# Kernel tuning notes

Measured on AMD Instinct MI355X. Metric: run time of the kernel, lower is better.

The kernel has to match this reference:

```python
import jax, jax.numpy as jnp
import numpy as np

K_SIM_SCHEDULE = [4, 8, 16]
K_CON_SCHEDULE = [2, 4, 8]
NEG = 1000000000.0


def _dual_adjacency(h, k_sim, k_con):
    """Binary causal dual adjacency (similar / dissimilar), no gradient."""
    B, T, D = h.shape
    h = jax.lax.stop_gradient(h)
    xn = h / jnp.maximum(jnp.linalg.norm(h, axis=-1, keepdims=True), 1e-12)
    sim = jnp.einsum('btd,bsd->bts', xn, xn)                 # (B,T,T)
    past = jnp.tril(jnp.ones((T, T), h.dtype), -1)           # strictly-past mask
    sim = sim * past - NEG * (1.0 - past)
    eff_sim = min(k_sim, T - 1)
    eff_con = min(k_con, max(0, T - 1 - eff_sim))
    bI = jnp.arange(B)[:, None, None]
    tI = jnp.arange(T)[None, :, None]
    A_sim = jnp.zeros((B, T, T), h.dtype)
    if eff_sim > 0:
        _, top_idx = jax.lax.top_k(sim, eff_sim)             # (B,T,k)
        A_sim = A_sim.at[bI, tI, top_idx].set(1.0) * past
    A_con = jnp.zeros((B, T, T), h.dtype)
    if eff_con > 0:
        sim_con = jnp.where(A_sim > 0, NEG, sim)
        _, bot_idx = jax.lax.top_k(-sim_con, eff_con)        # smallest eff_con
        A_con = A_con.at[bI, tI, bot_idx].set(1.0) * past * (1.0 - A_sim)
    return A_sim, A_con


def _aggregate(h, A):
    # unweighted mean over selected neighbors; empty rows -> zeros
    deg = jnp.sum(A, axis=-1, keepdims=True)
    return jnp.einsum('bts,bsd->btd', A, h) / jnp.maximum(deg, 1.0)


def setup_inputs() -> dict:
    key = jax.random.key(0)
    ks = jax.random.split(key, 2)
    B, T, D, R = 4, 2048, 512, 3
    x = jax.random.normal(ks[0], (B, T, D), dtype=jnp.float32)
    gain = jnp.ones((R, D), dtype=jnp.float32)
    bias = jnp.zeros((R, D), dtype=jnp.float32)
    log_mix = jnp.zeros((R,), dtype=jnp.float32)
    log_alpha = jnp.zeros((R,), dtype=jnp.float32)
    log_momentum = jnp.asarray(1.0, dtype=jnp.float32)
    log_scale = jnp.asarray(0.0, dtype=jnp.float32)
    return {"x": x, "gain": gain, "bias": bias, "log_mix": log_mix,
            "log_alpha": log_alpha, "log_momentum": log_momentum,
            "log_scale": log_scale}


def reference(x, gain, bias, log_mix, log_alpha, log_momentum, log_scale):
    momentum = jax.nn.sigmoid(log_momentum)
    scale = jax.nn.softplus(log_scale) + 0.01
    h = x
    for r in range(len(K_SIM_SCHEDULE)):
        mix = jax.nn.sigmoid(log_mix[r])
        alpha = jax.nn.sigmoid(log_alpha[r])
        A_sim, A_con = _dual_adjacency(h, K_SIM_SCHEDULE[r], K_CON_SCHEDULE[r])
        msg_pos = _aggregate(h, A_sim)
        msg_neg = _aggregate(h, A_con)
        ctx = alpha * msg_pos + (1.0 - alpha) * msg_neg
        blended = mix * h + (1.0 - mix) * ctx
        h_new = jax.nn.gelu(blended * gain[r] + bias[r], approximate=False)
        h = momentum * h + (1.0 - momentum) * h_new
    return (h - x) * scale
```

## Files before the change

### kernel.cpp

```cpp
#include <hip/hip_runtime.h>
#include <hip/hip_bf16.h>
#include <cstdint>
#include <cstddef>

#define BB 4
#define TT 2048
#define DD 512
#define NEG_INF (-3.402823466e+38f)
#define POS_INF (3.402823466e+38f)

typedef __attribute__((ext_vector_type(8))) short bf16x8;
typedef __attribute__((ext_vector_type(8))) unsigned short ushort8;
typedef __attribute__((ext_vector_type(4))) float f32x4;

__device__ __forceinline__ float sigmoidf_(float x){ return 1.0f/(1.0f+expf(-x)); }

__device__ __forceinline__ unsigned short f2bf(float x){
  __hip_bfloat16 b = __float2bfloat16(x);
  return *reinterpret_cast<unsigned short*>(&b);
}

__device__ __forceinline__ unsigned int fwd_map(float f){
  unsigned int b = __float_as_uint(f);
  return b ^ ((b & 0x80000000u) ? 0xFFFFFFFFu : 0x80000000u);
}
__device__ __forceinline__ float inv_map(unsigned int u){
  unsigned int b = (u & 0x80000000u) ? (u ^ 0x80000000u) : ~u;
  return __uint_as_float(b);
}

__device__ __forceinline__ unsigned long long shfl_xor64(unsigned long long x, int off){
  unsigned int hi = __shfl_xor((unsigned int)(x >> 32), off);
  unsigned int lo = __shfl_xor((unsigned int)x, off);
  return ((unsigned long long)hi << 32) | lo;
}

__global__ __launch_bounds__(64) void k_normsplit(const float* __restrict__ h, float* __restrict__ rnorm,
                                                  unsigned short* __restrict__ Xh, unsigned short* __restrict__ Xl){
  int row = blockIdx.x;
  const float* hr = h + (size_t)row*DD;
  int lane = threadIdx.x;
  float4 v0 = *(const float4*)&hr[lane*4];
  float4 v1 = *(const float4*)&hr[lane*4 + 256];
  float ss = v0.x*v0.x+v0.y*v0.y+v0.z*v0.z+v0.w*v0.w
           + v1.x*v1.x+v1.y*v1.y+v1.z*v1.z+v1.w*v1.w;
  #pragma unroll
  for (int off=32; off; off>>=1) ss += __shfl_xor(ss, off);
  float rn = 1.0f / fmaxf(sqrtf(ss), 1e-12f);
  if (lane==0) rnorm[row] = rn;

  float xs[8] = {v0.x,v0.y,v0.z,v0.w,v1.x,v1.y,v1.z,v1.w};
  unsigned short hb[8], lb[8];
  #pragma unroll
  for (int q=0;q<8;q++){
    float xn = xs[q]*rn;
    unsigned short hh = f2bf(xn);
    __hip_bfloat16 bh = *reinterpret_cast<__hip_bfloat16*>(&hh);
    float rem = xn - __bfloat162float(bh);
    hb[q] = hh; lb[q] = f2bf(rem);
  }
  ushort4 h0 = {hb[0],hb[1],hb[2],hb[3]}, h1 = {hb[4],hb[5],hb[6],hb[7]};
  ushort4 l0 = {lb[0],lb[1],lb[2],lb[3]}, l1 = {lb[4],lb[5],lb[6],lb[7]};
  *(ushort4*)&Xh[(size_t)row*DD + lane*4]       = h0;
  *(ushort4*)&Xh[(size_t)row*DD + lane*4 + 256] = h1;
  *(ushort4*)&Xl[(size_t)row*DD + lane*4]       = l0;
  *(ushort4*)&Xl[(size_t)row*DD + lane*4 + 256] = l1;
}

__global__ __launch_bounds__(256) void k_sim(const unsigned short* __restrict__ Xh,
                                             const unsigned short* __restrict__ Xl,
                                             float* __restrict__ sim, int b0){
  int p = blockIdx.x;
  int jt = (int)((sqrtf(8.0f*(float)p + 1.0f) - 1.0f)*0.5f);
  while ((jt+1)*(jt+2)/2 <= p) jt++;
  while (jt*(jt+1)/2 > p) jt--;
  int is = p - jt*(jt+1)/2;

  int bl = blockIdx.y;
  size_t xoff = (size_t)(b0 + bl)*TT*DD;
  const unsigned short* XhB = Xh + xoff;
  const unsigned short* XlB = Xl + xoff;
  float* simb = sim + (size_t)bl*TT*TT;
  int t0 = jt*128, s0 = is*128;

  __shared__ __align__(16) short As[128*32];
  __shared__ __align__(16) short Bs[128*32];

  int tid = threadIdx.x, wave = tid>>6, lane = tid&63;
  int wr = wave>>1, wc = wave&1;

  int srow = tid>>2;
  int sc8  = (tid&3)*8;

  f32x4 acc[4][4];
  #pragma unroll
  for (int m=0;m<4;m++)
    #pragma unroll
    for (int n=0;n<4;n++) acc[m][n] = (f32x4){0.f,0.f,0.f,0.f};

  ushort8 ra0, ra1, rb0, rb1;
  auto gload = [&](int s){
    int pass = s>>4; int kcol = (s&15)*32;
    const unsigned short* sA = (pass<2) ? XhB : XlB;
    const unsigned short* sB = (pass!=1) ? XhB : XlB;
    ra0 = *(const ushort8*)&sA[(size_t)(t0+srow)*DD + kcol + sc8];
    ra1 = *(const ushort8*)&sA[(size_t)(t0+srow+64)*DD + kcol + sc8];
    rb0 = *(const ushort8*)&sB[(size_t)(s0+srow)*DD + kcol + sc8];
    rb1 = *(const ushort8*)&sB[(size_t)(s0+srow+64)*DD + kcol + sc8];
  };

  gload(0);
  for (int s=0; s<48; ++s){
    __syncthreads();
    *(ushort8*)&As[srow*32 + sc8]      = ra0;
    *(ushort8*)&As[(srow+64)*32 + sc8] = ra1;
    *(ushort8*)&Bs[srow*32 + sc8]      = rb0;
    *(ushort8*)&Bs[(srow+64)*32 + sc8] = rb1;
    __syncthreads();
    if (s < 47) gload(s+1);

    int arow = wr*64 + (lane&15);
    int brow = wc*64 + (lane&15);
    int kb = (lane>>4)*8;
    bf16x8 af[4], bf[4];
    #pragma unroll
    for (int m=0;m<4;m++) af[m] = *(const bf16x8*)&As[(arow + m*16)*32 + kb];
    #pragma unroll
    for (int n=0;n<4;n++) bf[n] = *(const bf16x8*)&Bs[(brow + n*16)*32 + kb];
    #pragma unroll
    for (int m=0;m<4;m++)
      #pragma unroll
      for (int n=0;n<4;n++)
        acc[m][n] = __builtin_amdgcn_mfma_f32_16x16x32_bf16(af[m], bf[n], acc[m][n], 0, 0, 0);
  }

  #pragma unroll
  for (int m=0;m<4;m++){
    int t = t0 + wr*64 + m*16 + (lane>>4)*4;
    #pragma unroll
    for (int n=0;n<4;n++){
      int sc = s0 + wc*64 + n*16 + (lane&15);
      float* dst = simb + (size_t)t*TT + sc;
      #pragma unroll
      for (int j=0;j<4;j++) dst[(size_t)j*TT] = acc[m][n][j];
    }
  }
}

#define BMASK 0xFFFFFF00u

__device__ __forceinline__ unsigned int radix24(const float* __restrict__ srow, int t, int k1,
                                                unsigned int flip, int* sh, int lane){
  #pragma unroll
  for (int i=0;i<4;i++) sh[lane + i*64] = 0;
  int t4 = t & ~3;
  for (int s4 = lane*4; s4 < t4; s4 += 256){
    float4 f = *(const float4*)&srow[s4];
    unsigned int u0=fwd_map(f.x)^flip, u1=fwd_map(f.y)^flip, u2=fwd_map(f.z)^flip, u3=fwd_map(f.w)^flip;
    atomicAdd(&sh[u0>>24],1); atomicAdd(&sh[u1>>24],1);
    atomicAdd(&sh[u2>>24],1); atomicAdd(&sh[u3>>24],1);
  }
  for (int s = t4 + lane; s < t; s += 64){
    unsigned int u = fwd_map(srow[s])^flip;
    atomicAdd(&sh[u>>24],1);
  }
  unsigned int pfx = 0u; int kp = k1;
  #pragma unroll
  for (int pass = 0; pass < 3; ++pass){
    int shift = 24 - 8*pass;
    int m4 = sh[4*lane] + sh[4*lane+1] + sh[4*lane+2] + sh[4*lane+3];
    int x = __shfl(m4, 63-lane);
    #pragma unroll
    for (int off = 1; off < 64; off <<= 1){
      int v = __shfl_up(x, off);
      if (lane >= off) x += v;
    }
    int T = __shfl(x, 63-lane);
    int G = T - m4;
    bool hit = (G < kp) && (kp <= T);
    unsigned int npfx = 0u; int nkp = 0;
    if (hit){
      int c = G; int D = 4*lane;
      #pragma unroll
      for (int i = 3; i >= 0; --i){
        int hc = sh[4*lane + i];
        if (kp <= c + hc){ D = 4*lane + i; break; }
        c += hc;
      }
      npfx = pfx | ((unsigned int)D << shift);
      nkp = kp - c;
    }
    unsigned long long hm = __ballot(hit);
    int src = __ffsll(hm) - 1;
    pfx = __shfl(npfx, src);
    kp  = __shfl(nkp, src);
    if (pass == 2) break;

    int nshift = shift - 8;
    unsigned int keep = 0xFFFFFFFFu << shift;
    #pragma unroll
    for (int i=0;i<4;i++) sh[lane + i*64] = 0;
    for (int s4 = lane*4; s4 < t4; s4 += 256){
      float4 f = *(const float4*)&srow[s4];
      unsigned int u0=fwd_map(f.x)^flip, u1=fwd_map(f.y)^flip, u2=fwd_map(f.z)^flip, u3=fwd_map(f.w)^flip;
      if (((u0 ^ pfx) & keep) == 0) atomicAdd(&sh[(u0>>nshift)&255],1);
      if (((u1 ^ pfx) & keep) == 0) atomicAdd(&sh[(u1>>nshift)&255],1);
      if (((u2 ^ pfx) & keep) == 0) atomicAdd(&sh[(u2>>nshift)&255],1);
      if (((u3 ^ pfx) & keep) == 0) atomicAdd(&sh[(u3>>nshift)&255],1);
    }
    for (int s = t4 + lane; s < t; s += 64){
      unsigned int u = fwd_map(srow[s])^flip;
      if (((u ^ pfx) & keep) == 0) atomicAdd(&sh[(u>>nshift)&255],1);
    }
  }
  return pfx;
}

template<int ESIM, int ECON>
__global__ __launch_bounds__(256) void k_topk(const float* __restrict__ sim, int b0,
                                              const float* __restrict__ h, const float* __restrict__ rnorm,
                                              int* __restrict__ topidx, int* __restrict__ botidx,
                                              int* __restrict__ bcnt){
  constexpr int K1  = ESIM + 8;
  constexpr int K1B = ESIM + ECON + 8;
  constexpr int CANDCAP = 40;
  constexpr int EQCAP = 44;
  constexpr float TAU = 5e-5f;
  __shared__ int s_hist[4][256];
  __shared__ int s_cand[4][CANDCAP];
  __shared__ int s_eq[4][EQCAP];
  __shared__ int s_sel[4][ESIM];
  __shared__ int s_bot[4][16];
  __shared__ int s_cnt[4][2];

  int tid = threadIdx.x, lane = tid & 63, wid = tid >> 6;
  int lrow = blockIdx.x*4 + wid;
  int bl = lrow >> 11, t = lrow & (TT-1);
  int gb = b0 + bl;
  int grow = (gb << 11) | t;

  if (t <= ESIM){
    if (lane < t) topidx[(size_t)grow*16 + lane] = lane;
    if (lane == 0) bcnt[grow] = 0;
    return;
  }
  const float* srow = sim + (size_t)lrow*TT;
  const float* hb  = h + (size_t)gb*TT*DD;
  const float* rnb = rnorm + (size_t)gb*TT;

  int* sh    = s_hist[wid];
  int* scand = s_cand[wid];
  int* seq   = s_eq[wid];
  int* ssel  = s_sel[wid];
  int* sbot  = s_bot[wid];
  int t4 = t & ~3;

  unsigned long long kv0=0, kv1=0, kv2=0, kv3=0;
  {
    #define MKKEY(F,S) ((((unsigned long long)fwd_map(F)) << 32) | (unsigned int)(~(S)))
    #define INS(KK) do{ unsigned long long a=(KK); \
      if (a > kv3){ \
        if (a > kv0){ unsigned long long tq=kv0; kv0=a; a=tq; } \
        if (a > kv1){ unsigned long long tq=kv1; kv1=a; a=tq; } \
        if (a > kv2){ unsigned long long tq=kv2; kv2=a; a=tq; } \
        kv3=a; } }while(0)
    for (int s4 = lane*4; s4 < t4; s4 += 256){
      float4 f = *(const float4*)&srow[s4];
      INS(MKKEY(f.x,s4)); INS(MKKEY(f.y,s4+1)); INS(MKKEY(f.z,s4+2)); INS(MKKEY(f.w,s4+3));
    }
    for (int s = t4 + lane; s < t; s += 64) INS(MKKEY(srow[s],s));
  }

  int myidx = 0x7fffffff;
  float vA = 0.f, vB = 0.f;
  unsigned long long keyLast = 0ull;
  #pragma unroll
  for (int k = 0; k <= ESIM; ++k){
    unsigned long long bk = kv0;
    #pragma unroll
    for (int off=32; off; off>>=1){
      unsigned long long ok = shfl_xor64(bk, off);
      if (ok > bk) bk = ok;
    }
    if (kv0 == bk){ kv0=kv1; kv1=kv2; kv2=kv3; kv3=0ull; }
    if (lane == k) myidx = (int)(~(unsigned int)bk);
    if (k == ESIM-1) vA = inv_map((unsigned int)(bk >> 32));
    if (k == ESIM){ vB = inv_map((unsigned int)(bk >> 32)); keyLast = bk; }
  }

  int cnt = 0;
  for (int s4 = lane*4; s4 < t4; s4 += 256){
    float4 f = *(const float4*)&srow[s4];
    cnt += (MKKEY(f.x,s4)   > keyLast);
    cnt += (MKKEY(f.y,s4+1) > keyLast);
    cnt += (MKKEY(f.z,s4+2) > keyLast);
    cnt += (MKKEY(f.w,s4+3) > keyLast);
  }
  for (int s = t4 + lane; s < t; s += 64) cnt += (MKKEY(srow[s],s) > keyLast);
  #pragma unroll
  for (int off=32; off; off>>=1) cnt += __shfl_xor(cnt, off);

  bool fb = (cnt != ESIM) || (vA - vB < TAU);
  if (!fb){
    if (lane < ESIM){
      ssel[lane] = myidx;
      topidx[(size_t)grow*16 + lane] = myidx;
    }
  } else {
    int k1 = min(t, K1);
    unsigned int thr = radix24(srow, t, k1, 0u, sh, lane);

    if (lane == 0){ s_cnt[wid][0] = 0; s_cnt[wid][1] = 0; }
    for (int s4 = lane*4; s4 < t4; s4 += 256){
      float4 f = *(const float4*)&srow[s4];
      unsigned int uu[4] = {fwd_map(f.x), fwd_map(f.y), fwd_map(f.z), fwd_map(f.w)};
      #pragma unroll
      for (int q=0;q<4;q++){
        unsigned int b24 = uu[q] & BMASK;
        if (b24 > thr){ int p = atomicAdd(&s_cnt[wid][0],1); if (p < CANDCAP) scand[p] = s4+q; }
        else if (b24 == thr){ int p = atomicAdd(&s_cnt[wid][1],1); if (p < EQCAP) seq[p] = s4+q; }
      }
    }
    for (int s = t4 + lane; s < t; s += 64){
      unsigned int b24 = fwd_map(srow[s]) & BMASK;
      if (b24 > thr){ int p = atomicAdd(&s_cnt[wid][0],1); if (p < CANDCAP) scand[p] = s; }
      else if (b24 == thr){ int p = atomicAdd(&s_cnt[wid][1],1); if (p < EQCAP) seq[p] = s; }
    }
    int c_gt = min(s_cnt[wid][0], CANDCAP);
    int c_eq = min(s_cnt[wid][1], EQCAP);
    int ncand = min(c_gt + c_eq, 64);

    unsigned int myu = 0u; int myi = 0x7fffffff;
    if (lane < ncand){
      myi = (lane < c_gt) ? scand[lane] : seq[lane - c_gt];
      myu = fwd_map(srow[myi]);
    }

    float fvA = 0.f, fvB = 0.f;
    {
      unsigned int cu = myu; int ci = myi;
      #pragma unroll
      for (int k = 0; k <= ESIM; ++k){
        unsigned int bu = cu; int bi = ci;
        #pragma unroll
        for (int off=32; off; off>>=1){
          unsigned int ou = __shfl_xor(bu, off); int oi = __shfl_xor(bi, off);
          if (ou > bu || (ou == bu && oi < bi)){ bu = ou; bi = oi; }
        }
        if (k < ESIM && lane == 0) ssel[k] = bi;
        if (k == ESIM-1) fvA = inv_map(bu);
        if (k == ESIM)   fvB = inv_map(bu);
        if (ci == bi){ cu = 0u; ci = 0x7fffffff; }
      }
    }

    bool resc = (fvA - fvB < TAU);
    if (resc){
      const float* hq = hb + (size_t)t*DD;
      float rt = rnb[t];
      float4 q0 = *(const float4*)&hq[lane*4];
      float4 q1 = *(const float4*)&hq[lane*4 + 256];
      float ev = NEG_INF;
      for (int j = 0; j < ncand; ++j){
        int idx = (j < c_gt) ? scand[j] : seq[j - c_gt];
        const float* hc = hb + (size_t)idx*DD;
        float4 c0 = *(const float4*)&hc[lane*4];
        float4 c1 = *(const float4*)&hc[lane*4 + 256];
        float pp = q0.x*c0.x+q0.y*c0.y+q0.z*c0.z+q0.w*c0.w
                 + q1.x*c1.x+q1.y*c1.y+q1.z*c1.z+q1.w*c1.w;
        #pragma unroll
        for (int off=32; off; off>>=1) pp += __shfl_xor(pp, off);
        float ex = pp * rt * rnb[idx];
        if (lane == j) ev = ex;
      }
      float rv = (lane < ncand) ? ev : NEG_INF;
      int   ri = myi;
      #pragma unroll
      for (int k = 0; k < ESIM; ++k){
        float bv = rv; int bi = ri;
        #pragma unroll
        for (int off=32; off; off>>=1){
          float ov = __shfl_xor(bv, off); int oi = __shfl_xor(bi, off);
          if (ov > bv || (ov == bv && oi < bi)){ bv = ov; bi = oi; }
        }
        if (lane == 0) ssel[k] = bi;
        if (ri == bi) rv = NEG_INF;
      }
    }
    if (lane < ESIM) topidx[(size_t)grow*16 + lane] = ssel[lane];
  }

  int need = ECON - (TT - t);
  int cnt2 = 0;
  if (need > 0){
    constexpr unsigned int FLIP = 0xFFFFFFFFu;
    int k1b = min(t, K1B);
    unsigned int thrb = radix24(srow, t, k1b, FLIP, sh, lane);

    if (lane == 0){ s_cnt[wid][0] = 0; s_cnt[wid][1] = 0; }
    for (int s4 = lane*4; s4 < t4; s4 += 256){
      float4 f = *(const float4*)&srow[s4];
      unsigned int uu[4] = {fwd_map(f.x)^FLIP, fwd_map(f.y)^FLIP, fwd_map(f.z)^FLIP, fwd_map(f.w)^FLIP};
      #pragma unroll
      for (int q=0;q<4;q++){
        unsigned int b24 = uu[q] & BMASK;
        if (b24 > thrb){ int p = atomicAdd(&s_cnt[wid][0],1); if (p < CANDCAP) scand[p] = s4+q; }
        else if (b24 == thrb){ int p = atomicAdd(&s_cnt[wid][1],1); if (p < EQCAP) seq[p] = s4+q; }
      }
    }
    for (int s = t4 + lane; s < t; s += 64){
      unsigned int u = fwd_map(srow[s])^FLIP;
      unsigned int b24 = u & BMASK;
      if (b24 > thrb){ int p = atomicAdd(&s_cnt[wid][0],1); if (p < CANDCAP) scand[p] = s; }
      else if (b24 == thrb){ int p = atomicAdd(&s_cnt[wid][1],1); if (p < EQCAP) seq[p] = s; }
    }
    int bc_gt = min(s_cnt[wid][0], CANDCAP);
    int bc_eq = min(s_cnt[wid][1], EQCAP);
    int ncb = min(bc_gt + bc_eq, 64);

    unsigned int mu = 0u; int mi = 0x7fffffff;
    if (lane < ncb){
      mi = (lane < bc_gt) ? scand[lane] : seq[lane - bc_gt];
      mu = fwd_map(srow[mi]) ^ FLIP;
    }
    float wA = 0.f, wB = 0.f;
    unsigned int cu = mu; int ci = mi;
    #pragma unroll
    for (int k = 0; k < K1B; ++k){
      if (k < ncb && cnt2 < need + 8){
        unsigned int bu = cu; int bi = ci;
        #pragma unroll
        for (int off=32; off; off>>=1){
          unsigned int ou = __shfl_xor(bu, off); int oi = __shfl_xor(bi, off);
          if (ou > bu || (ou == bu && oi < bi)){ bu = ou; bi = oi; }
        }
        if (ci == bi){ cu = 0u; ci = 0x7fffffff; }
        bool mem = false;
        #pragma unroll
        for (int j=0;j<ESIM;j++) if (ssel[j] == bi) mem = true;
        if (!mem){
          if (lane == 0) sbot[cnt2] = bi;
          float val = inv_map(bu ^ FLIP);
          if (cnt2 == need-1) wA = val;
          if (cnt2 == need)   wB = val;
          cnt2++;
        }
      }
    }
    int npick = min(need, cnt2);
    bool rb = (cnt2 > need) && (wB - wA < TAU);
    if (!rb){
      if (lane < npick) botidx[(size_t)grow*8 + lane] = sbot[lane];
    } else {
      const float* hq = hb + (size_t)t*DD;
      float rt = rnb[t];
      float4 q0 = *(const float4*)&hq[lane*4];
      float4 q1 = *(const float4*)&hq[lane*4 + 256];
      float ev = POS_INF; int ei = 0x7fffffff;
      for (int j = 0; j < cnt2; ++j){
        int idx = sbot[j];
        const float* hc = hb + (size_t)idx*DD;
        float4 c0 = *(const float4*)&hc[lane*4];
        float4 c1 = *(const float4*)&hc[lane*4 + 256];
        float pp = q0.x*c0.x+q0.y*c0.y+q0.z*c0.z+q0.w*c0.w
                 + q1.x*c1.x+q1.y*c1.y+q1.z*c1.z+q1.w*c1.w;
        #pragma unroll
        for (int off=32; off; off>>=1) pp += __shfl_xor(pp, off);
        float ex = pp * rt * rnb[idx];
        if (lane == j){ ev = ex; ei = idx; }
      }
      #pragma unroll
      for (int k = 0; k < ECON; ++k){
        if (k < npick){
          float bv = ev; int bi = ei;
          #pragma unroll
          for (int off=32; off; off>>=1){
            float ov = __shfl_xor(bv, off); int oi = __shfl_xor(bi, off);
            if (ov < bv || (ov == bv && oi < bi)){ bv = ov; bi = oi; }
          }
          if (lane == 0) botidx[(size_t)grow*8 + k] = bi;
          if (ei == bi) ev = POS_INF;
        }
      }
    }
    cnt2 = npick;
  }
  if (lane == 0) bcnt[grow] = cnt2;
}

__global__ __launch_bounds__(256) void k_agg(const float* __restrict__ hsrc, float* __restrict__ hdst,
                                             const int* __restrict__ topidx, const int* __restrict__ botidx,
                                             const int* __restrict__ bcnt,
                                             const float* __restrict__ gain, const float* __restrict__ bias,
                                             const float* __restrict__ log_mix, const float* __restrict__ log_alpha,
                                             const float* __restrict__ log_momentum, int r, int eff_sim){
  int row = blockIdx.x;
  int b = row >> 11; int t = row & (TT-1);
  int n_sim = min(eff_sim, t);
  int n_con = bcnt[row];
  float mix      = sigmoidf_(log_mix[r]);
  float alpha    = sigmoidf_(log_alpha[r]);
  float momentum = sigmoidf_(log_momentum[0]);
  const float* hb = hsrc + (size_t)b*TT*DD;

  __shared__ int sidx[16];
  __shared__ int scidx[8];
  if (threadIdx.x < 16) sidx[threadIdx.x]  = (threadIdx.x < n_sim) ? topidx[(size_t)row*16 + threadIdx.x] : 0;
  if (threadIdx.x < 8)  scidx[threadIdx.x] = (threadIdx.x < n_con) ? botidx[(size_t)row*8  + threadIdx.x] : 0;
  __syncthreads();

  #pragma unroll
  for (int e = threadIdx.x; e < DD; e += 256){
    float sp = 0.f;
    for (int j=0;j<n_sim;j++) sp += hb[(size_t)sidx[j]*DD + e];
    float sn = 0.f;
    for (int j=0;j<n_con;j++) sn += hb[(size_t)scidx[j]*DD + e];
    float mp = sp / (float)max(n_sim, 1);
    float mn = sn / (float)max(n_con, 1);
    float ctx = alpha*mp + (1.f-alpha)*mn;
    float hv = hsrc[(size_t)row*DD + e];
    float blended = mix*hv + (1.f-mix)*ctx;
    float u = blended*gain[e] + bias[e];
    float g = 0.5f*u*(1.0f + erff(u*0.7071067811865475f));
    hdst[(size_t)row*DD + e] = momentum*hv + (1.f-momentum)*g;
  }
}

__global__ __launch_bounds__(256) void k_final(const float* __restrict__ hfin, const float* __restrict__ x,
                                               const float* __restrict__ log_scale, float* __restrict__ out, int n){
  float scale = log1pf(expf(log_scale[0])) + 0.01f;
  int i = blockIdx.x*256 + threadIdx.x;
  if (i < n) out[i] = (hfin[i] - x[i]) * scale;
}

extern "C" void kernel_launch(void* const* d_in, const int* in_sizes, int n_in,
                              void* d_out, int out_size, void* d_ws, size_t ws_size,
                              hipStream_t stream) {
  const float* x         = (const float*)d_in[0];
  const float* gain      = (const float*)d_in[1];
  const float* bias      = (const float*)d_in[2];
  const float* log_mix   = (const float*)d_in[3];
  const float* log_alpha = (const float*)d_in[4];
  const float* log_mom   = (const float*)d_in[5];
  const float* log_scale = (const float*)d_in[6];

  float* hA = (float*)d_out;
  char* ws = (char*)d_ws;
  size_t off = 0;
  auto alloc = [&](size_t bytes){ void* p = ws + off; off += (bytes + 255) & ~(size_t)255; return p; };

  float*          hB     = (float*)alloc((size_t)BB*TT*DD*4);
  float*          rnorm  = (float*)alloc((size_t)BB*TT*4);
  int*            topidx = (int*)  alloc((size_t)BB*TT*16*4);
  int*            botidx = (int*)  alloc((size_t)BB*TT*8*4);
  int*            bcnt   = (int*)  alloc((size_t)BB*TT*4);
  unsigned short* Xh     = (unsigned short*)alloc((size_t)BB*TT*DD*2);
  unsigned short* Xl     = (unsigned short*)alloc((size_t)BB*TT*DD*2);

  size_t rem = (ws_size > off) ? (ws_size - off) : 0;
  int cb = (int)(rem / ((size_t)TT*TT*4));
  if (cb < 1) cb = 1;
  if (cb > BB) cb = BB;
  float* sim = (float*)alloc((size_t)cb*TT*TT*4);

  const float* hsrc = x;
  float* hdst = hB;
  const int ks[3] = {4, 8, 16};

  for (int r = 0; r < 3; ++r){
    k_normsplit<<<BB*TT, 64, 0, stream>>>(hsrc, rnorm, Xh, Xl);
    for (int b0 = 0; b0 < BB; b0 += cb){
      int nb = (BB - b0 < cb) ? (BB - b0) : cb;
      dim3 g(136, nb);
      k_sim<<<g, 256, 0, stream>>>(Xh, Xl, sim, b0);
      if (r == 0)      k_topk<4,2><<<nb*TT/4, 256, 0, stream>>>(sim, b0, hsrc, rnorm, topidx, botidx, bcnt);
      else if (r == 1) k_topk<8,4><<<nb*TT/4, 256, 0, stream>>>(sim, b0, hsrc, rnorm, topidx, botidx, bcnt);
      else             k_topk<16,8><<<nb*TT/4, 256, 0, stream>>>(sim, b0, hsrc, rnorm, topidx, botidx, bcnt);
    }
    k_agg<<<BB*TT, 256, 0, stream>>>(hsrc, hdst, topidx, botidx, bcnt,
                                     gain + (size_t)r*DD, bias + (size_t)r*DD,
                                     log_mix, log_alpha, log_mom, r, ks[r]);
    if (r == 0){ hsrc = hB; hdst = hA; }
    else if (r == 1){ hsrc = hA; hdst = hB; }
  }
  k_final<<<(BB*TT*DD)/256, 256, 0, stream>>>(hB, x, log_scale, (float*)d_out, BB*TT*DD);
}
```

Before: 462.9 us.

## Process each top-k row with a full 256-thread block instead of one wave

The top-k kernel now assigns one similarity row per block, with all four waves scanning the row for the candidate pass and the verification count. Each wave publishes its local top-(k+1) keys to shared memory, wave 0 merges them, and the count is combined through a shared atomic. The fallback radix path and the bottom-k selection remain single-wave, so the other three waves sit idle there. This adds block-wide syncs and launches four times as many blocks in exchange for shorter per-row scan latency.

```diff
diff --git a/kernel.cpp b/kernel.cpp
--- a/kernel.cpp
+++ b/kernel.cpp
@@ -148,6 +148,13 @@
 }
 
 #define BMASK 0xFFFFFF00u
+#define MKKEY(F,S) ((((unsigned long long)fwd_map(F)) << 32) | (unsigned int)(~(S)))
+#define INS(KK) do{ unsigned long long a=(KK); \
+  if (a > kv3){ \
+    if (a > kv0){ unsigned long long tq=kv0; kv0=a; a=tq; } \
+    if (a > kv1){ unsigned long long tq=kv1; kv1=a; a=tq; } \
+    if (a > kv2){ unsigned long long tq=kv2; kv2=a; a=tq; } \
+    kv3=a; } }while(0)
 
 __device__ __forceinline__ unsigned int radix24(const float* __restrict__ srow, int t, int k1,
                                                 unsigned int flip, int* sh, int lane){
@@ -225,57 +232,46 @@
   constexpr int K1B = ESIM + ECON + 8;
   constexpr int CANDCAP = 40;
   constexpr int EQCAP = 44;
+  constexpr int NP = ESIM + 1;
   constexpr float TAU = 5e-5f;
-  __shared__ int s_hist[4][256];
-  __shared__ int s_cand[4][CANDCAP];
-  __shared__ int s_eq[4][EQCAP];
-  __shared__ int s_sel[4][ESIM];
-  __shared__ int s_bot[4][16];
-  __shared__ int s_cnt[4][2];
+
+  __shared__ unsigned long long s_keys[4*NP];
+  __shared__ unsigned long long s_keyLast;
+  __shared__ int s_cntTot;
+  __shared__ int s_hist[256];
+  __shared__ int s_cand[CANDCAP];
+  __shared__ int s_eq[EQCAP];
+  __shared__ int s_sel[ESIM];
+  __shared__ int s_bot[16];
+  __shared__ int s_cnt[2];
 
   int tid = threadIdx.x, lane = tid & 63, wid = tid >> 6;
-  int lrow = blockIdx.x*4 + wid;
+  int lrow = blockIdx.x;
   int bl = lrow >> 11, t = lrow & (TT-1);
   int gb = b0 + bl;
   int grow = (gb << 11) | t;
 
   if (t <= ESIM){
-    if (lane < t) topidx[(size_t)grow*16 + lane] = lane;
-    if (lane == 0) bcnt[grow] = 0;
+    if (tid < t) topidx[(size_t)grow*16 + tid] = tid;
+    if (tid == 0) bcnt[grow] = 0;
     return;
   }
   const float* srow = sim + (size_t)lrow*TT;
   const float* hb  = h + (size_t)gb*TT*DD;
   const float* rnb = rnorm + (size_t)gb*TT;
-
-  int* sh    = s_hist[wid];
-  int* scand = s_cand[wid];
-  int* seq   = s_eq[wid];
-  int* ssel  = s_sel[wid];
-  int* sbot  = s_bot[wid];
   int t4 = t & ~3;
 
+  if (tid == 0) s_cntTot = 0;
+
   unsigned long long kv0=0, kv1=0, kv2=0, kv3=0;
-  {
-    #define MKKEY(F,S) ((((unsigned long long)fwd_map(F)) << 32) | (unsigned int)(~(S)))
-    #define INS(KK) do{ unsigned long long a=(KK); \
-      if (a > kv3){ \
-        if (a > kv0){ unsigned long long tq=kv0; kv0=a; a=tq; } \
-        if (a > kv1){ unsigned long long tq=kv1; kv1=a; a=tq; } \
-        if (a > kv2){ unsigned long long tq=kv2; kv2=a; a=tq; } \
-        kv3=a; } }while(0)
-    for (int s4 = lane*4; s4 < t4; s4 += 256){
-      float4 f = *(const float4*)&srow[s4];
-      INS(MKKEY(f.x,s4)); INS(MKKEY(f.y,s4+1)); INS(MKKEY(f.z,s4+2)); INS(MKKEY(f.w,s4+3));
-    }
-    for (int s = t4 + lane; s < t; s += 64) INS(MKKEY(srow[s],s));
-  }
-
-  int myidx = 0x7fffffff;
-  float vA = 0.f, vB = 0.f;
-  unsigned long long keyLast = 0ull;
-  #pragma unroll
-  for (int k = 0; k <= ESIM; ++k){
+  for (int s4 = tid*4; s4 < t4; s4 += 1024){
+    float4 f = *(const float4*)&srow[s4];
+    INS(MKKEY(f.x,s4)); INS(MKKEY(f.y,s4+1)); INS(MKKEY(f.z,s4+2)); INS(MKKEY(f.w,s4+3));
+  }
+  for (int s = t4 + tid; s < t; s += 256) INS(MKKEY(srow[s],s));
+
+  #pragma unroll
+  for (int k = 0; k < NP; ++k){
     unsigned long long bk = kv0;
     #pragma unroll
     for (int off=32; off; off>>=1){
@@ -283,24 +279,61 @@
       if (ok > bk) bk = ok;
     }
     if (kv0 == bk){ kv0=kv1; kv1=kv2; kv2=kv3; kv3=0ull; }
-    if (lane == k) myidx = (int)(~(unsigned int)bk);
-    if (k == ESIM-1) vA = inv_map((unsigned int)(bk >> 32));
-    if (k == ESIM){ vB = inv_map((unsigned int)(bk >> 32)); keyLast = bk; }
-  }
-
-  int cnt = 0;
-  for (int s4 = lane*4; s4 < t4; s4 += 256){
-    float4 f = *(const float4*)&srow[s4];
-    cnt += (MKKEY(f.x,s4)   > keyLast);
-    cnt += (MKKEY(f.y,s4+1) > keyLast);
-    cnt += (MKKEY(f.z,s4+2) > keyLast);
-    cnt += (MKKEY(f.w,s4+3) > keyLast);
-  }
-  for (int s = t4 + lane; s < t; s += 64) cnt += (MKKEY(srow[s],s) > keyLast);
-  #pragma unroll
-  for (int off=32; off; off>>=1) cnt += __shfl_xor(cnt, off);
-
-  bool fb = (cnt != ESIM) || (vA - vB < TAU);
+    if (lane == 0) s_keys[wid*NP + k] = bk;
+  }
+  __syncthreads();
+
+  int myidx = 0x7fffffff;
+  float vA = 0.f, vB = 0.f;
+  if (wid == 0){
+    constexpr int NL = 4*NP;
+    unsigned long long m0 = (lane < NL) ? s_keys[lane] : 0ull;
+    unsigned long long m1 = (lane + 64 < NL) ? s_keys[lane + 64] : 0ull;
+    if (m1 > m0){ unsigned long long tq=m0; m0=m1; m1=tq; }
+    unsigned long long keyLast = 0ull;
+    #pragma unroll
+    for (int k = 0; k < NP; ++k){
+      unsigned long long bk = m0;
+      #pragma unroll
+      for (int off=32; off; off>>=1){
+        unsigned long long ok = shfl_xor64(bk, off);
+        if (ok > bk) bk = ok;
+      }
+      if (m0 == bk){ m0 = m1; m1 = 0ull; }
+      if (lane == k) myidx = (int)(~(unsigned int)bk);
+      if (k == ESIM-1) vA = inv_map((unsigned int)(bk >> 32));
+      if (k == ESIM){ vB = inv_map((unsigned int)(bk >> 32)); keyLast = bk; }
+    }
+    if (lane == 0) s_keyLast = keyLast;
+  }
+  __syncthreads();
+
+  {
+    unsigned long long kL = s_keyLast;
+    int cnt = 0;
+    for (int s4 = tid*4; s4 < t4; s4 += 1024){
+      float4 f = *(const float4*)&srow[s4];
+      cnt += (MKKEY(f.x,s4)   > kL);
+      cnt += (MKKEY(f.y,s4+1) > kL);
+      cnt += (MKKEY(f.z,s4+2) > kL);
+      cnt += (MKKEY(f.w,s4+3) > kL);
+    }
+    for (int s = t4 + tid; s < t; s += 256) cnt += (MKKEY(srow[s],s) > kL);
+    #pragma unroll
+    for (int off=32; off; off>>=1) cnt += __shfl_xor(cnt, off);
+    if (lane == 0) atomicAdd(&s_cntTot, cnt);
+  }
+  __syncthreads();
+
+  if (wid != 0) return;
+
+  int* sh    = s_hist;
+  int* scand = s_cand;
+  int* seq   = s_eq;
+  int* ssel  = s_sel;
+  int* sbot  = s_bot;
+
+  bool fb = (s_cntTot != ESIM) || (vA - vB < TAU);
   if (!fb){
     if (lane < ESIM){
       ssel[lane] = myidx;
@@ -310,24 +343,24 @@
     int k1 = min(t, K1);
     unsigned int thr = radix24(srow, t, k1, 0u, sh, lane);
 
-    if (lane == 0){ s_cnt[wid][0] = 0; s_cnt[wid][1] = 0; }
+    if (lane == 0){ s_cnt[0] = 0; s_cnt[1] = 0; }
     for (int s4 = lane*4; s4 < t4; s4 += 256){
       float4 f = *(const float4*)&srow[s4];
       unsigned int uu[4] = {fwd_map(f.x), fwd_map(f.y), fwd_map(f.z), fwd_map(f.w)};
       #pragma unroll
       for (int q=0;q<4;q++){
         unsigned int b24 = uu[q] & BMASK;
-        if (b24 > thr){ int p = atomicAdd(&s_cnt[wid][0],1); if (p < CANDCAP) scand[p] = s4+q; }
-        else if (b24 == thr){ int p = atomicAdd(&s_cnt[wid][1],1); if (p < EQCAP) seq[p] = s4+q; }
+        if (b24 > thr){ int p = atomicAdd(&s_cnt[0],1); if (p < CANDCAP) scand[p] = s4+q; }
+        else if (b24 == thr){ int p = atomicAdd(&s_cnt[1],1); if (p < EQCAP) seq[p] = s4+q; }
       }
     }
     for (int s = t4 + lane; s < t; s += 64){
       unsigned int b24 = fwd_map(srow[s]) & BMASK;
-      if (b24 > thr){ int p = atomicAdd(&s_cnt[wid][0],1); if (p < CANDCAP) scand[p] = s; }
-      else if (b24 == thr){ int p = atomicAdd(&s_cnt[wid][1],1); if (p < EQCAP) seq[p] = s; }
-    }
-    int c_gt = min(s_cnt[wid][0], CANDCAP);
-    int c_eq = min(s_cnt[wid][1], EQCAP);
+      if (b24 > thr){ int p = atomicAdd(&s_cnt[0],1); if (p < CANDCAP) scand[p] = s; }
+      else if (b24 == thr){ int p = atomicAdd(&s_cnt[1],1); if (p < EQCAP) seq[p] = s; }
+    }
+    int c_gt = min(s_cnt[0], CANDCAP);
+    int c_eq = min(s_cnt[1], EQCAP);
     int ncand = min(c_gt + c_eq, 64);
 
     unsigned int myu = 0u; int myi = 0x7fffffff;
@@ -397,25 +430,25 @@
     int k1b = min(t, K1B);
     unsigned int thrb = radix24(srow, t, k1b, FLIP, sh, lane);
 
-    if (lane == 0){ s_cnt[wid][0] = 0; s_cnt[wid][1] = 0; }
+    if (lane == 0){ s_cnt[0] = 0; s_cnt[1] = 0; }
     for (int s4 = lane*4; s4 < t4; s4 += 256){
       float4 f = *(const float4*)&srow[s4];
       unsigned int uu[4] = {fwd_map(f.x)^FLIP, fwd_map(f.y)^FLIP, fwd_map(f.z)^FLIP, fwd_map(f.w)^FLIP};
       #pragma unroll
       for (int q=0;q<4;q++){
         unsigned int b24 = uu[q] & BMASK;
-        if (b24 > thrb){ int p = atomicAdd(&s_cnt[wid][0],1); if (p < CANDCAP) scand[p] = s4+q; }
-        else if (b24 == thrb){ int p = atomicAdd(&s_cnt[wid][1],1); if (p < EQCAP) seq[p] = s4+q; }
+        if (b24 > thrb){ int p = atomicAdd(&s_cnt[0],1); if (p < CANDCAP) scand[p] = s4+q; }
+        else if (b24 == thrb){ int p = atomicAdd(&s_cnt[1],1); if (p < EQCAP) seq[p] = s4+q; }
       }
     }
     for (int s = t4 + lane; s < t; s += 64){
       unsigned int u = fwd_map(srow[s])^FLIP;
       unsigned int b24 = u & BMASK;
-      if (b24 > thrb){ int p = atomicAdd(&s_cnt[wid][0],1); if (p < CANDCAP) scand[p] = s; }
-      else if (b24 == thrb){ int p = atomicAdd(&s_cnt[wid][1],1); if (p < EQCAP) seq[p] = s; }
-    }
-    int bc_gt = min(s_cnt[wid][0], CANDCAP);
-    int bc_eq = min(s_cnt[wid][1], EQCAP);
+      if (b24 > thrb){ int p = atomicAdd(&s_cnt[0],1); if (p < CANDCAP) scand[p] = s; }
+      else if (b24 == thrb){ int p = atomicAdd(&s_cnt[1],1); if (p < EQCAP) seq[p] = s; }
+    }
+    int bc_gt = min(s_cnt[0], CANDCAP);
+    int bc_eq = min(s_cnt[1], EQCAP);
     int ncb = min(bc_gt + bc_eq, 64);
 
     unsigned int mu = 0u; int mi = 0x7fffffff;
@@ -573,9 +606,9 @@
       int nb = (BB - b0 < cb) ? (BB - b0) : cb;
       dim3 g(136, nb);
       k_sim<<<g, 256, 0, stream>>>(Xh, Xl, sim, b0);
-      if (r == 0)      k_topk<4,2><<<nb*TT/4, 256, 0, stream>>>(sim, b0, hsrc, rnorm, topidx, botidx, bcnt);
-      else if (r == 1) k_topk<8,4><<<nb*TT/4, 256, 0, stream>>>(sim, b0, hsrc, rnorm, topidx, botidx, bcnt);
-      else             k_topk<16,8><<<nb*TT/4, 256, 0, stream>>>(sim, b0, hsrc, rnorm, topidx, botidx, bcnt);
+      if (r == 0)      k_topk<4,2><<<nb*TT, 256, 0, stream>>>(sim, b0, hsrc, rnorm, topidx, botidx, bcnt);
+      else if (r == 1) k_topk<8,4><<<nb*TT, 256, 0, stream>>>(sim, b0, hsrc, rnorm, topidx, botidx, bcnt);
+      else             k_topk<16,8><<<nb*TT, 256, 0, stream>>>(sim, b0, hsrc, rnorm, topidx, botidx, bcnt);
     }
     k_agg<<<BB*TT, 256, 0, stream>>>(hsrc, hdst, topidx, botidx, bcnt,
                                      gain + (size_t)r*DD, bias + (size_t)r*DD,
```

Measured after the change: 576.5 us. 24.5% more time.
